# Optimization experiments

Measured on AMD Instinct MI355X. Metric: run time of the kernel, lower is better.

The kernel has to match this reference:

```python
import jax, jax.numpy as jnp
import numpy as np

N = 20000
E = 160000
H = 8          # heads
D = 96         # head_dim (768 // 8)
C = H * D      # 768 hidden channels
G = 256        # num graphs
NUM_CLASSES = 32
SLOPE = 0.2    # GATv2 LeakyReLU negative slope


def layer_norm(x, w, b, eps=1e-5):
    mu = jnp.mean(x, axis=-1, keepdims=True)
    var = jnp.mean(jnp.square(x - mu), axis=-1, keepdims=True)
    return (x - mu) * jax.lax.rsqrt(var + eps) * w + b


def gatv2_layer(x, src, dst, Wl, bl, Wr, br, att, bias):
    # x: [N, C]; src/dst: [E'] with self loops included
    xl = (x @ Wl + bl).reshape(N, H, D)   # source projection
    xr = (x @ Wr + br).reshape(N, H, D)   # target projection
    e = xl[src] + xr[dst]                 # [E', H, D] edge gather
    e = jnp.where(e > 0, e, SLOPE * e)    # LeakyReLU
    logits = jnp.einsum('ehd,hd->eh', e, att)  # [E', H]
    m = jax.ops.segment_max(logits, dst, num_segments=N)
    ex = jnp.exp(logits - m[dst])
    s = jax.ops.segment_sum(ex, dst, num_segments=N)
    alpha = ex / s[dst]                   # segment softmax over in-edges
    out = jax.ops.segment_sum(alpha[:, :, None] * xl[src], dst, num_segments=N)
    return out.reshape(N, C) + bias


def setup_inputs() -> dict:
    key = jax.random.key(0)
    ks = jax.random.split(key, 24)
    x = jax.random.normal(ks[0], (N, 768), jnp.float32)
    edge_index = jax.random.randint(ks[1], (2, E), 0, N, jnp.int64)
    batch = jnp.sort(jax.random.randint(ks[2], (N,), 0, G, jnp.int64))
    sc = 1.0 / np.sqrt(C)
    p = {
        'x': x, 'edge_index': edge_index, 'batch': batch,
        'w_in': jax.random.normal(ks[3], (768, C), jnp.float32) * sc,
        'b_in': jnp.zeros((C,), jnp.float32),
        'Wl': jax.random.normal(ks[4], (3, C, C), jnp.float32) * sc,
        'bl': jnp.zeros((3, C), jnp.float32),
        'Wr': jax.random.normal(ks[5], (3, C, C), jnp.float32) * sc,
        'br': jnp.zeros((3, C), jnp.float32),
        'att': jax.random.normal(ks[6], (3, H, D), jnp.float32) * (1.0 / np.sqrt(D)),
        'gat_bias': jnp.zeros((3, C), jnp.float32),
        'ln_w': jnp.ones((3, C), jnp.float32),
        'ln_b': jnp.zeros((3, C), jnp.float32),
        'out_ln_w': jnp.ones((3 * C,), jnp.float32),
        'out_ln_b': jnp.zeros((3 * C,), jnp.float32),
        'w_out': jax.random.normal(ks[7], (3 * C, NUM_CLASSES), jnp.float32) * (1.0 / np.sqrt(3 * C)),
        'b_out': jnp.zeros((NUM_CLASSES,), jnp.float32),
    }
    return p


def reference(x, edge_index, batch, w_in, b_in, Wl, bl, Wr, br, att, gat_bias,
              ln_w, ln_b, out_ln_w, out_ln_b, w_out, b_out):
    # add self loops (PyG add_self_loops=True)
    loops = jnp.arange(N, dtype=edge_index.dtype)
    src = jnp.concatenate([edge_index[0], loops])
    dst = jnp.concatenate([edge_index[1], loops])

    h = x @ w_in + b_in
    jumps = []
    for l in range(3):
        a = gatv2_layer(h, src, dst, Wl[l], bl[l], Wr[l], br[l], att[l], gat_bias[l])
        h = layer_norm(a + h, ln_w[l], ln_b[l])
        h = jax.nn.gelu(h, approximate=False)
        jumps.append(h)
    hc = jnp.concatenate(jumps, axis=-1)  # JumpingKnowledge 'cat' -> [N, 3C]

    # global mean pool over graphs
    sums = jax.ops.segment_sum(hc, batch, num_segments=G)
    cnt = jax.ops.segment_sum(jnp.ones((N, 1), hc.dtype), batch, num_segments=G)
    pooled = sums / jnp.maximum(cnt, 1.0)

    out = layer_norm(pooled, out_ln_w, out_ln_b)
    return out @ w_out + b_out
```

## Files before the change

### kernel.cpp

```cpp
#include <hip/hip_runtime.h>

#define N_NODES 20000
#define N_EDGES 160000
#define CH      768
#define CH3     2304
#define NGRAPH  256
#define NCLS    32

typedef __bf16 bf16v8 __attribute__((ext_vector_type(8)));
typedef float  f32x4  __attribute__((ext_vector_type(4)));

__device__ __forceinline__ float b2f(ushort u) {
    union { float f; unsigned u; } x; x.u = ((unsigned)u) << 16; return x.f;
}
__device__ __forceinline__ ushort f2b(float f) {
    union { float f; unsigned u; } x; x.f = f;
    unsigned r = x.u + 0x7FFFu + ((x.u >> 16) & 1u);
    return (ushort)(r >> 16);
}
__device__ __forceinline__ void load12(const ushort* __restrict__ p, float* o) {
    const ushort4* q = (const ushort4*)p;
    ushort4 a = q[0], b = q[1], c = q[2];
    o[0]=b2f(a.x); o[1]=b2f(a.y); o[2]=b2f(a.z); o[3]=b2f(a.w);
    o[4]=b2f(b.x); o[5]=b2f(b.y); o[6]=b2f(b.z); o[7]=b2f(b.w);
    o[8]=b2f(c.x); o[9]=b2f(c.y); o[10]=b2f(c.z); o[11]=b2f(c.w);
}
__device__ __forceinline__ void load12f(const float* __restrict__ p, float* o) {
    const float4* q = (const float4*)p;
    float4 a = q[0], b = q[1], c = q[2];
    o[0]=a.x; o[1]=a.y; o[2]=a.z; o[3]=a.w;
    o[4]=b.x; o[5]=b.y; o[6]=b.z; o[7]=b.w;
    o[8]=c.x; o[9]=c.y; o[10]=c.z; o[11]=c.w;
}
__device__ __forceinline__ void async_copy16(void* lds, const void* gp) {
    __builtin_amdgcn_global_load_lds((const void __attribute__((address_space(1)))*)gp,
                                     (void __attribute__((address_space(3)))*)lds, 16, 0, 0);
}

__global__ void cvt_x_kernel(const float* __restrict__ src, ushort* __restrict__ dst, int n4) {
    int i = blockIdx.x * 256 + threadIdx.x;
    if (i >= n4) return;
    float4 v = ((const float4*)src)[i];
    ushort4 o; o.x = f2b(v.x); o.y = f2b(v.y); o.z = f2b(v.z); o.w = f2b(v.w);
    ((ushort4*)dst)[i] = o;
}

__global__ void transpose_cvt_all(const float* __restrict__ w_in,
                                  const float* __restrict__ Wl,
                                  const float* __restrict__ Wr,
                                  ushort* __restrict__ wt_in,
                                  ushort* __restrict__ wt_l) {
    __shared__ float tile[32][33];
    int z = blockIdx.z;
    const float* in;
    ushort* out;
    if (z == 0) { in = w_in; out = wt_in; }
    else {
        int l = (z - 1) >> 1, isr = (z - 1) & 1;
        in  = (isr ? Wr : Wl) + (size_t)l * CH * CH;
        out = wt_l + (size_t)l * 1536 * CH + (size_t)isr * CH * CH;
    }
    int bx = blockIdx.x * 32, by = blockIdx.y * 32;
    int tx = threadIdx.x, ty = threadIdx.y;
    #pragma unroll
    for (int i = ty; i < 32; i += 8) tile[i][tx] = in[(size_t)(by + i) * CH + bx + tx];
    __syncthreads();
    #pragma unroll
    for (int i = ty; i < 32; i += 8) out[(size_t)(bx + i) * CH + by + tx] = f2b(tile[tx][i]);
}

__global__ void init_kernel(int* deg, int* gcount, int n) {
    int i = blockIdx.x * 256 + threadIdx.x;
    if (i < n) deg[i] = 1;
    if (i < 256) gcount[i] = 0;
}
__global__ void count_both_kernel(const int* __restrict__ dst, int* __restrict__ deg, int e,
                                  const int* __restrict__ batch, int* __restrict__ gcount, int n) {
    int i = blockIdx.x * 256 + threadIdx.x;
    if (i < e) atomicAdd(&deg[dst[i]], 1);
    if (i < n) atomicAdd(&gcount[batch[i]], 1);
}
__global__ __launch_bounds__(1024) void scan_kernel(const int* __restrict__ deg,
                                                    int* __restrict__ rowptr, int n) {
    __shared__ int part[1024];
    int t = threadIdx.x;
    const int chunk = (n + 1023) / 1024;
    int base = t * chunk;
    int s = 0;
    for (int i = 0; i < chunk; ++i) { int idx = base + i; if (idx < n) s += deg[idx]; }
    part[t] = s; __syncthreads();
    for (int off = 1; off < 1024; off <<= 1) {
        int v = (t >= off) ? part[t - off] : 0;
        __syncthreads();
        part[t] += v;
        __syncthreads();
    }
    int run = (t == 0) ? 0 : part[t - 1];
    for (int i = 0; i < chunk; ++i) {
        int idx = base + i;
        if (idx < n) { rowptr[idx] = run; run += deg[idx]; }
    }
    if (t == 1023) rowptr[n] = part[1023];
}
__global__ void selfloop_kernel(const int* __restrict__ rowptr, int* __restrict__ csrc,
                                int* __restrict__ cursor, int n) {
    int i = blockIdx.x * 256 + threadIdx.x;
    if (i < n) { int p = rowptr[i]; csrc[p] = i; cursor[i] = p + 1; }
}
__global__ void scatter_kernel(const int* __restrict__ src, const int* __restrict__ dst,
                               int* __restrict__ cursor, int* __restrict__ csrc, int e) {
    int i = blockIdx.x * 256 + threadIdx.x;
    if (i < e) { int p = atomicAdd(&cursor[dst[i]], 1); csrc[p] = src[i]; }
}
__global__ __launch_bounds__(256) void gscan_kernel(const int* __restrict__ gcount,
                                                    int* __restrict__ gstart) {
    __shared__ int p[256];
    int t = threadIdx.x;
    p[t] = gcount[t]; __syncthreads();
    for (int off = 1; off < 256; off <<= 1) {
        int v = (t >= off) ? p[t - off] : 0;
        __syncthreads();
        p[t] += v;
        __syncthreads();
    }
    gstart[t] = p[t] - gcount[t];
    if (t == 255) gstart[256] = p[255];
}

__global__ __launch_bounds__(256) void gemm_bf16_kernel(
    const ushort* __restrict__ A, int lda,
    const ushort* __restrict__ Bt,
    const float* __restrict__ biasA, const float* __restrict__ biasB, int nsplit,
    ushort* __restrict__ C, int ldc, int M) {
    __shared__ __bf16 As[128 * 32];
    __shared__ __bf16 Bs[128 * 32];
    int tid = threadIdx.x;
    int wave = tid >> 6, lane = tid & 63;
    int wr = wave >> 1, wc = wave & 1;

    int bid = blockIdx.y * gridDim.x + blockIdx.x;
    int pf = 8 * gridDim.y;
    int p  = bid / pf;
    int rem = bid - p * pf;
    int rp = min(8, (int)gridDim.x - p * 8);
    int row_t = p * 8 + rem % rp;
    int col_t = rem / rp;
    int row0 = row_t * 128, col0 = col_t * 128;

    int c1 = wave * 64 + lane, c2 = c1 + 256;
    int ar1 = min(row0 + (c1 >> 2), M - 1), ak1 = (c1 & 3) * 8;
    int ar2 = min(row0 + (c2 >> 2), M - 1), ak2 = (c2 & 3) * 8;
    int br1 = col0 + (c1 >> 2), br2 = col0 + (c2 >> 2);
    const ushort* a1 = A + (size_t)ar1 * lda + ak1;
    const ushort* a2 = A + (size_t)ar2 * lda + ak2;
    const ushort* b1 = Bt + (size_t)br1 * CH + ak1;
    const ushort* b2 = Bt + (size_t)br2 * CH + ak2;
    __bf16* asb1 = As + (wave * 64) * 8;
    __bf16* asb2 = As + (256 + wave * 64) * 8;
    __bf16* bsb1 = Bs + (wave * 64) * 8;
    __bf16* bsb2 = Bs + (256 + wave * 64) * 8;

    f32x4 acc[4][4] = {};
    int l16 = lane & 15, lq = lane >> 4;

    for (int k0 = 0; k0 < CH; k0 += 32) {
        async_copy16(asb1, a1 + k0);
        async_copy16(asb2, a2 + k0);
        async_copy16(bsb1, b1 + k0);
        async_copy16(bsb2, b2 + k0);
        __syncthreads();
        bf16v8 av[4], bv[4];
        #pragma unroll
        for (int i = 0; i < 4; ++i)
            av[i] = *(const bf16v8*)(As + ((wr * 64 + i * 16 + l16) * 32 + lq * 8));
        #pragma unroll
        for (int j = 0; j < 4; ++j)
            bv[j] = *(const bf16v8*)(Bs + ((wc * 64 + j * 16 + l16) * 32 + lq * 8));
        #pragma unroll
        for (int i = 0; i < 4; ++i)
            #pragma unroll
            for (int j = 0; j < 4; ++j)
                acc[i][j] = __builtin_amdgcn_mfma_f32_16x16x32_bf16(av[i], bv[j], acc[i][j], 0, 0, 0);
        __syncthreads();
    }
    #pragma unroll
    for (int i = 0; i < 4; ++i) {
        int mbase = row0 + wr * 64 + i * 16 + lq * 4;
        #pragma unroll
        for (int j = 0; j < 4; ++j) {
            int col = col0 + wc * 64 + j * 16 + l16;
            float bb = (col < nsplit) ? biasA[col] : biasB[col - nsplit];
            #pragma unroll
            for (int r = 0; r < 4; ++r) {
                int mm = mbase + r;
                if (mm < M) C[(size_t)mm * ldc + col] = f2b(acc[i][j][r] + bb);
            }
        }
    }
}

__global__ __launch_bounds__(256) void gat_node_kernel(
    const ushort* __restrict__ xlxr,
    const ushort* __restrict__ hin, int ldh,
    const int* __restrict__ rowptr, const int* __restrict__ csrc,
    const float* __restrict__ att, const float* __restrict__ gbias,
    const float* __restrict__ lnw, const float* __restrict__ lnb,
    ushort* __restrict__ hout, int nn) {
    int wv = threadIdx.x >> 6, lane = threadIdx.x & 63;
    int n = blockIdx.x * 4 + wv;
    if (n >= nn) return;
    int c0 = lane * 12;
    float attv[12], xr[12], acc1[12], acc2[12];
    load12f(att + c0, attv);
    load12(xlxr + (size_t)n * 1536 + CH + c0, xr);
    #pragma unroll
    for (int j = 0; j < 12; ++j) { acc1[j] = 0.f; acc2[j] = 0.f; }
    float m1 = -1e30f, s1 = 0.f, m2 = -1e30f, s2 = 0.f;
    int rs = rowptr[n], re = rowptr[n + 1];
    int e = rs;
    for (; e + 1 < re; e += 2) {
        int sa = csrc[e], sb = csrc[e + 1];
        float xa[12], xb[12];
        load12(xlxr + (size_t)sa * 1536 + c0, xa);
        load12(xlxr + (size_t)sb * 1536 + c0, xb);
        float da = 0.f, db = 0.f;
        #pragma unroll
        for (int j = 0; j < 12; ++j) {
            float va = xa[j] + xr[j]; va = (va > 0.f) ? va : 0.2f * va;
            float vb = xb[j] + xr[j]; vb = (vb > 0.f) ? vb : 0.2f * vb;
            da = fmaf(va, attv[j], da);
            db = fmaf(vb, attv[j], db);
        }
        da += __shfl_xor(da, 1); db += __shfl_xor(db, 1);
        da += __shfl_xor(da, 2); db += __shfl_xor(db, 2);
        da += __shfl_xor(da, 4); db += __shfl_xor(db, 4);
        float nm1 = fmaxf(m1, da), nm2 = fmaxf(m2, db);
        float sc1 = __expf(m1 - nm1), sc2 = __expf(m2 - nm2);
        float ex1 = __expf(da - nm1), ex2 = __expf(db - nm2);
        s1 = s1 * sc1 + ex1;
        s2 = s2 * sc2 + ex2;
        #pragma unroll
        for (int j = 0; j < 12; ++j) {
            acc1[j] = fmaf(acc1[j], sc1, ex1 * xa[j]);
            acc2[j] = fmaf(acc2[j], sc2, ex2 * xb[j]);
        }
        m1 = nm1; m2 = nm2;
    }
    if (e < re) {
        int sa = csrc[e];
        float xa[12];
        load12(xlxr + (size_t)sa * 1536 + c0, xa);
        float da = 0.f;
        #pragma unroll
        for (int j = 0; j < 12; ++j) {
            float va = xa[j] + xr[j]; va = (va > 0.f) ? va : 0.2f * va;
            da = fmaf(va, attv[j], da);
        }
        da += __shfl_xor(da, 1);
        da += __shfl_xor(da, 2);
        da += __shfl_xor(da, 4);
        float nm = fmaxf(m1, da);
        float sc = __expf(m1 - nm), ex = __expf(da - nm);
        s1 = s1 * sc + ex;
        #pragma unroll
        for (int j = 0; j < 12; ++j) acc1[j] = fmaf(acc1[j], sc, ex * xa[j]);
        m1 = nm;
    }
    float M = fmaxf(m1, m2);
    float w1 = __expf(m1 - M), w2 = __expf(m2 - M);
    float ssum = s1 * w1 + s2 * w2;
    float inv = 1.f / ssum;
    float hres[12], gb[12], tv[12];
    load12(hin + (size_t)n * ldh + c0, hres);
    load12f(gbias + c0, gb);
    float lsum = 0.f;
    #pragma unroll
    for (int j = 0; j < 12; ++j) {
        tv[j] = (acc1[j] * w1 + acc2[j] * w2) * inv + gb[j] + hres[j];
        lsum += tv[j];
    }
    #pragma unroll
    for (int o = 1; o < 64; o <<= 1) lsum += __shfl_xor(lsum, o);
    float mu = lsum * (1.f / 768.f);
    float lsq = 0.f;
    #pragma unroll
    for (int j = 0; j < 12; ++j) { float d = tv[j] - mu; lsq = fmaf(d, d, lsq); }
    #pragma unroll
    for (int o = 1; o < 64; o <<= 1) lsq += __shfl_xor(lsq, o);
    float rstd = rsqrtf(lsq * (1.f / 768.f) + 1e-5f);
    float wv12[12], bv12[12];
    load12f(lnw + c0, wv12);
    load12f(lnb + c0, bv12);
    ushort* op = hout + (size_t)n * CH3 + c0;
    #pragma unroll
    for (int j = 0; j < 12; ++j) {
        float y = (tv[j] - mu) * rstd * wv12[j] + bv12[j];
        float g = 0.5f * y * (1.f + erff(y * 0.70710678118f));
        op[j] = f2b(g);
    }
}

__global__ __launch_bounds__(256) void pool_kernel(const ushort* __restrict__ hc,
                                                   const int* __restrict__ gstart,
                                                   float* __restrict__ pooled) {
    int g = blockIdx.x;
    int c = blockIdx.y * 256 + threadIdx.x;
    int s = gstart[g], e = gstart[g + 1];
    const ushort* p = hc + (size_t)s * CH3 + c;
    float a = 0.f;
    for (int n = s; n < e; ++n) { a += b2f(*p); p += CH3; }
    pooled[(size_t)g * CH3 + c] = a * (1.f / (float)max(e - s, 1));
}

__global__ __launch_bounds__(256) void head_kernel(const float* __restrict__ pooled,
                                                   const float* __restrict__ olnw,
                                                   const float* __restrict__ olnb,
                                                   const float* __restrict__ wout,
                                                   const float* __restrict__ bout,
                                                   float* __restrict__ outp) {
    __shared__ float row[CH3];
    __shared__ float red[8];
    __shared__ float parts[8][32];
    int g = blockIdx.x, t = threadIdx.x;
    int lane = t & 63, wv = t >> 6;
    float s = 0.f;
    for (int c = t; c < CH3; c += 256) { float v = pooled[(size_t)g * CH3 + c]; row[c] = v; s += v; }
    #pragma unroll
    for (int o = 1; o < 64; o <<= 1) s += __shfl_xor(s, o);
    if (lane == 0) red[wv] = s;
    __syncthreads();
    float mu = (red[0] + red[1] + red[2] + red[3]) * (1.f / (float)CH3);
    float q = 0.f;
    for (int c = t; c < CH3; c += 256) { float d = row[c] - mu; q += d * d; }
    #pragma unroll
    for (int o = 1; o < 64; o <<= 1) q += __shfl_xor(q, o);
    if (lane == 0) red[4 + wv] = q;
    __syncthreads();
    float rstd = rsqrtf((red[4] + red[5] + red[6] + red[7]) * (1.f / (float)CH3) + 1e-5f);
    for (int c = t; c < CH3; c += 256)
        row[c] = (row[c] - mu) * rstd * olnw[c] + olnb[c];
    __syncthreads();
    int j = t & 31, slice = t >> 5;
    float a = 0.f;
    int cb = slice * (CH3 / 8);
    for (int c = cb; c < cb + CH3 / 8; ++c) a += row[c] * wout[(size_t)c * 32 + j];
    parts[slice][j] = a;
    __syncthreads();
    if (t < 32) {
        float r = bout[t];
        #pragma unroll
        for (int si = 0; si < 8; ++si) r += parts[si][t];
        outp[(size_t)g * 32 + t] = r;
    }
}

extern "C" void kernel_launch(void* const* d_in, const int* in_sizes, int n_in,
                              void* d_out, int out_size, void* d_ws, size_t ws_size,
                              hipStream_t stream) {
    const float* x     = (const float*)d_in[0];
    const int*   ei    = (const int*)d_in[1];
    const int*   batch = (const int*)d_in[2];
    const float* w_in  = (const float*)d_in[3];
    const float* b_in  = (const float*)d_in[4];
    const float* Wl    = (const float*)d_in[5];
    const float* bl    = (const float*)d_in[6];
    const float* Wr    = (const float*)d_in[7];
    const float* br    = (const float*)d_in[8];
    const float* att   = (const float*)d_in[9];
    const float* gbias = (const float*)d_in[10];
    const float* lnw   = (const float*)d_in[11];
    const float* lnb   = (const float*)d_in[12];
    const float* olnw  = (const float*)d_in[13];
    const float* olnb  = (const float*)d_in[14];
    const float* wout  = (const float*)d_in[15];
    const float* bout  = (const float*)d_in[16];

    char* ws = (char*)d_ws;
    size_t off = 0;
    auto alloc = [&](size_t bytes) -> void* {
        void* p = ws + off;
        off = (off + bytes + 255) & ~(size_t)255;
        return p;
    };
    ushort* h0     = (ushort*)alloc((size_t)N_NODES * CH * 2);
    ushort* hc     = (ushort*)alloc((size_t)N_NODES * CH3 * 2);
    ushort* xlxr   = (ushort*)alloc((size_t)N_NODES * 1536 * 2);
    ushort* wt_in  = (ushort*)alloc((size_t)CH * CH * 2);
    ushort* wt_l   = (ushort*)alloc((size_t)3 * 1536 * CH * 2);
    int*    deg    = (int*)alloc((size_t)N_NODES * 4);
    int*    rowptr = (int*)alloc((size_t)(N_NODES + 1) * 4);
    int*    cursor = (int*)alloc((size_t)N_NODES * 4);
    int*    csrc   = (int*)alloc((size_t)(N_EDGES + N_NODES) * 4);
    int*    gcount = (int*)alloc(256 * 4);
    int*    gstart = (int*)alloc(257 * 4);
    float*  pooled = (float*)alloc((size_t)NGRAPH * CH3 * 4);
    if (off > ws_size) return;

    ushort* xc = hc;

    cvt_x_kernel<<<(N_NODES * CH / 4 + 255) / 256, 256, 0, stream>>>(x, xc, N_NODES * CH / 4);
    transpose_cvt_all<<<dim3(24, 24, 7), dim3(32, 8), 0, stream>>>(w_in, Wl, Wr, wt_in, wt_l);

    int nb = (N_NODES + 255) / 256, eb = (N_EDGES + 255) / 256;
    init_kernel<<<nb, 256, 0, stream>>>(deg, gcount, N_NODES);
    count_both_kernel<<<eb, 256, 0, stream>>>(ei + N_EDGES, deg, N_EDGES, batch, gcount, N_NODES);
    scan_kernel<<<1, 1024, 0, stream>>>(deg, rowptr, N_NODES);
    selfloop_kernel<<<nb, 256, 0, stream>>>(rowptr, csrc, cursor, N_NODES);
    scatter_kernel<<<eb, 256, 0, stream>>>(ei, ei + N_EDGES, cursor, csrc, N_EDGES);
    gscan_kernel<<<1, 256, 0, stream>>>(gcount, gstart);

    gemm_bf16_kernel<<<dim3(157, 6), 256, 0, stream>>>(
        xc, CH, wt_in, b_in, b_in, CH, h0, CH, N_NODES);

    for (int l = 0; l < 3; ++l) {
        const ushort* hprev = (l == 0) ? h0 : (hc + (size_t)(l - 1) * CH);
        int ldh = (l == 0) ? CH : CH3;
        gemm_bf16_kernel<<<dim3(157, 12), 256, 0, stream>>>(
            hprev, ldh, wt_l + (size_t)l * 1536 * CH,
            bl + (size_t)l * CH, br + (size_t)l * CH, CH,
            xlxr, 1536, N_NODES);
        gat_node_kernel<<<N_NODES / 4, 256, 0, stream>>>(
            xlxr, hprev, ldh, rowptr, csrc,
            att + (size_t)l * CH, gbias + (size_t)l * CH,
            lnw + (size_t)l * CH, lnb + (size_t)l * CH,
            hc + (size_t)l * CH, N_NODES);
    }

    pool_kernel<<<dim3(NGRAPH, CH3 / 256), 256, 0, stream>>>(hc, gstart, pooled);
    head_kernel<<<NGRAPH, 256, 0, stream>>>(pooled, olnw, olnb, wout, bout, (float*)d_out);
}
```

Baseline: 754.3 us.

## Split each GAT node across two wavefronts and unroll pooling accumulation

The GAT aggregation kernel now assigns two wavefronts per node, each handling 384 channels (6 per lane), and combines the LayerNorm sums through shared memory using a single-pass sum and sum-of-squares. The aim is more parallelism and latency hiding for the edge gathers, plus vectorized ushort2 stores. The pool kernel uses four independent accumulators to raise memory-level parallelism. The init kernel is replaced by memsets, with self-loop degrees counted via atomics. The one-pass variance is numerically less stable, and a block-wide barrier is added.

```diff
diff --git a/kernel.cpp b/kernel.cpp
--- a/kernel.cpp
+++ b/kernel.cpp
@@ -25,12 +25,17 @@
     o[4]=b2f(b.x); o[5]=b2f(b.y); o[6]=b2f(b.z); o[7]=b2f(b.w);
     o[8]=b2f(c.x); o[9]=b2f(c.y); o[10]=b2f(c.z); o[11]=b2f(c.w);
 }
-__device__ __forceinline__ void load12f(const float* __restrict__ p, float* o) {
-    const float4* q = (const float4*)p;
-    float4 a = q[0], b = q[1], c = q[2];
-    o[0]=a.x; o[1]=a.y; o[2]=a.z; o[3]=a.w;
-    o[4]=b.x; o[5]=b.y; o[6]=b.z; o[7]=b.w;
-    o[8]=c.x; o[9]=c.y; o[10]=c.z; o[11]=c.w;
+__device__ __forceinline__ void load6(const ushort* __restrict__ p, float* o) {
+    const ushort2* q = (const ushort2*)p;
+    ushort2 a = q[0], b = q[1], c = q[2];
+    o[0]=b2f(a.x); o[1]=b2f(a.y);
+    o[2]=b2f(b.x); o[3]=b2f(b.y);
+    o[4]=b2f(c.x); o[5]=b2f(c.y);
+}
+__device__ __forceinline__ void load6f(const float* __restrict__ p, float* o) {
+    const float2* q = (const float2*)p;
+    float2 a = q[0], b = q[1], c = q[2];
+    o[0]=a.x; o[1]=a.y; o[2]=b.x; o[3]=b.y; o[4]=c.x; o[5]=c.y;
 }
 __device__ __forceinline__ void async_copy16(void* lds, const void* gp) {
     __builtin_amdgcn_global_load_lds((const void __attribute__((address_space(1)))*)gp,
@@ -69,16 +74,11 @@
     for (int i = ty; i < 32; i += 8) out[(size_t)(bx + i) * CH + by + tx] = f2b(tile[tx][i]);
 }
 
-__global__ void init_kernel(int* deg, int* gcount, int n) {
-    int i = blockIdx.x * 256 + threadIdx.x;
-    if (i < n) deg[i] = 1;
-    if (i < 256) gcount[i] = 0;
-}
 __global__ void count_both_kernel(const int* __restrict__ dst, int* __restrict__ deg, int e,
                                   const int* __restrict__ batch, int* __restrict__ gcount, int n) {
     int i = blockIdx.x * 256 + threadIdx.x;
     if (i < e) atomicAdd(&deg[dst[i]], 1);
-    if (i < n) atomicAdd(&gcount[batch[i]], 1);
+    if (i < n) { atomicAdd(&deg[i], 1); atomicAdd(&gcount[batch[i]], 1); }
 }
 __global__ __launch_bounds__(1024) void scan_kernel(const int* __restrict__ deg,
                                                     int* __restrict__ rowptr, int n) {
@@ -206,26 +206,28 @@
     const float* __restrict__ att, const float* __restrict__ gbias,
     const float* __restrict__ lnw, const float* __restrict__ lnb,
     ushort* __restrict__ hout, int nn) {
+    __shared__ float sred[2][2][2];
     int wv = threadIdx.x >> 6, lane = threadIdx.x & 63;
-    int n = blockIdx.x * 4 + wv;
-    if (n >= nn) return;
-    int c0 = lane * 12;
-    float attv[12], xr[12], acc1[12], acc2[12];
-    load12f(att + c0, attv);
-    load12(xlxr + (size_t)n * 1536 + CH + c0, xr);
-    #pragma unroll
-    for (int j = 0; j < 12; ++j) { acc1[j] = 0.f; acc2[j] = 0.f; }
+    int slot = wv >> 1, half = wv & 1;
+    int n = blockIdx.x * 2 + slot;
+    int c0 = half * 384 + lane * 6;
+    const ushort* __restrict__ xbase = xlxr + c0;
+    float attv[6], xr[6], acc1[6], acc2[6];
+    load6f(att + c0, attv);
+    load6(xbase + (size_t)n * 1536 + CH, xr);
+    #pragma unroll
+    for (int j = 0; j < 6; ++j) { acc1[j] = 0.f; acc2[j] = 0.f; }
     float m1 = -1e30f, s1 = 0.f, m2 = -1e30f, s2 = 0.f;
     int rs = rowptr[n], re = rowptr[n + 1];
     int e = rs;
     for (; e + 1 < re; e += 2) {
         int sa = csrc[e], sb = csrc[e + 1];
-        float xa[12], xb[12];
-        load12(xlxr + (size_t)sa * 1536 + c0, xa);
-        load12(xlxr + (size_t)sb * 1536 + c0, xb);
+        float xa[6], xb[6];
+        load6(xbase + (size_t)sa * 1536, xa);
+        load6(xbase + (size_t)sb * 1536, xb);
         float da = 0.f, db = 0.f;
         #pragma unroll
-        for (int j = 0; j < 12; ++j) {
+        for (int j = 0; j < 6; ++j) {
             float va = xa[j] + xr[j]; va = (va > 0.f) ? va : 0.2f * va;
             float vb = xb[j] + xr[j]; vb = (vb > 0.f) ? vb : 0.2f * vb;
             da = fmaf(va, attv[j], da);
@@ -234,13 +236,14 @@
         da += __shfl_xor(da, 1); db += __shfl_xor(db, 1);
         da += __shfl_xor(da, 2); db += __shfl_xor(db, 2);
         da += __shfl_xor(da, 4); db += __shfl_xor(db, 4);
+        da += __shfl_xor(da, 8); db += __shfl_xor(db, 8);
         float nm1 = fmaxf(m1, da), nm2 = fmaxf(m2, db);
         float sc1 = __expf(m1 - nm1), sc2 = __expf(m2 - nm2);
         float ex1 = __expf(da - nm1), ex2 = __expf(db - nm2);
         s1 = s1 * sc1 + ex1;
         s2 = s2 * sc2 + ex2;
         #pragma unroll
-        for (int j = 0; j < 12; ++j) {
+        for (int j = 0; j < 6; ++j) {
             acc1[j] = fmaf(acc1[j], sc1, ex1 * xa[j]);
             acc2[j] = fmaf(acc2[j], sc2, ex2 * xb[j]);
         }
@@ -248,56 +251,62 @@
     }
     if (e < re) {
         int sa = csrc[e];
-        float xa[12];
-        load12(xlxr + (size_t)sa * 1536 + c0, xa);
+        float xa[6];
+        load6(xbase + (size_t)sa * 1536, xa);
         float da = 0.f;
         #pragma unroll
-        for (int j = 0; j < 12; ++j) {
+        for (int j = 0; j < 6; ++j) {
             float va = xa[j] + xr[j]; va = (va > 0.f) ? va : 0.2f * va;
             da = fmaf(va, attv[j], da);
         }
         da += __shfl_xor(da, 1);
         da += __shfl_xor(da, 2);
         da += __shfl_xor(da, 4);
+        da += __shfl_xor(da, 8);
         float nm = fmaxf(m1, da);
         float sc = __expf(m1 - nm), ex = __expf(da - nm);
         s1 = s1 * sc + ex;
         #pragma unroll
-        for (int j = 0; j < 12; ++j) acc1[j] = fmaf(acc1[j], sc, ex * xa[j]);
+        for (int j = 0; j < 6; ++j) acc1[j] = fmaf(acc1[j], sc, ex * xa[j]);
         m1 = nm;
     }
     float M = fmaxf(m1, m2);
     float w1 = __expf(m1 - M), w2 = __expf(m2 - M);
-    float ssum = s1 * w1 + s2 * w2;
-    float inv = 1.f / ssum;
-    float hres[12], gb[12], tv[12];
-    load12(hin + (size_t)n * ldh + c0, hres);
-    load12f(gbias + c0, gb);
-    float lsum = 0.f;
-    #pragma unroll
-    for (int j = 0; j < 12; ++j) {
+    float inv = 1.f / (s1 * w1 + s2 * w2);
+    float hres[6], gb[6], tv[6];
+    load6(hin + (size_t)n * ldh + c0, hres);
+    load6f(gbias + c0, gb);
+    float lsum = 0.f, lsq = 0.f;
+    #pragma unroll
+    for (int j = 0; j < 6; ++j) {
         tv[j] = (acc1[j] * w1 + acc2[j] * w2) * inv + gb[j] + hres[j];
         lsum += tv[j];
-    }
-    #pragma unroll
-    for (int o = 1; o < 64; o <<= 1) lsum += __shfl_xor(lsum, o);
-    float mu = lsum * (1.f / 768.f);
-    float lsq = 0.f;
-    #pragma unroll
-    for (int j = 0; j < 12; ++j) { float d = tv[j] - mu; lsq = fmaf(d, d, lsq); }
-    #pragma unroll
-    for (int o = 1; o < 64; o <<= 1) lsq += __shfl_xor(lsq, o);
-    float rstd = rsqrtf(lsq * (1.f / 768.f) + 1e-5f);
-    float wv12[12], bv12[12];
-    load12f(lnw + c0, wv12);
-    load12f(lnb + c0, bv12);
-    ushort* op = hout + (size_t)n * CH3 + c0;
-    #pragma unroll
-    for (int j = 0; j < 12; ++j) {
-        float y = (tv[j] - mu) * rstd * wv12[j] + bv12[j];
-        float g = 0.5f * y * (1.f + erff(y * 0.70710678118f));
-        op[j] = f2b(g);
-    }
+        lsq = fmaf(tv[j], tv[j], lsq);
+    }
+    #pragma unroll
+    for (int o = 1; o < 64; o <<= 1) { lsum += __shfl_xor(lsum, o); lsq += __shfl_xor(lsq, o); }
+    if (lane == 0) { sred[slot][0][half] = lsum; sred[slot][1][half] = lsq; }
+    __syncthreads();
+    float S = sred[slot][0][0] + sred[slot][0][1];
+    float Q = sred[slot][1][0] + sred[slot][1][1];
+    float mu = S * (1.f / 768.f);
+    float var = Q * (1.f / 768.f) - mu * mu;
+    float rstd = rsqrtf(var + 1e-5f);
+    float wv6[6], bv6[6];
+    load6f(lnw + c0, wv6);
+    load6f(lnb + c0, bv6);
+    float g[6];
+    #pragma unroll
+    for (int j = 0; j < 6; ++j) {
+        float y = (tv[j] - mu) * rstd * wv6[j] + bv6[j];
+        g[j] = 0.5f * y * (1.f + erff(y * 0.70710678118f));
+    }
+    ushort2* o2 = (ushort2*)(hout + (size_t)n * CH3 + c0);
+    ushort2 u0, u1, u2;
+    u0.x = f2b(g[0]); u0.y = f2b(g[1]);
+    u1.x = f2b(g[2]); u1.y = f2b(g[3]);
+    u2.x = f2b(g[4]); u2.y = f2b(g[5]);
+    o2[0] = u0; o2[1] = u1; o2[2] = u2;
 }
 
 __global__ __launch_bounds__(256) void pool_kernel(const ushort* __restrict__ hc,
@@ -307,8 +316,17 @@
     int c = blockIdx.y * 256 + threadIdx.x;
     int s = gstart[g], e = gstart[g + 1];
     const ushort* p = hc + (size_t)s * CH3 + c;
-    float a = 0.f;
-    for (int n = s; n < e; ++n) { a += b2f(*p); p += CH3; }
+    float a0 = 0.f, a1 = 0.f, a2 = 0.f, a3 = 0.f;
+    int n = s;
+    for (; n + 3 < e; n += 4) {
+        a0 += b2f(p[0]);
+        a1 += b2f(p[CH3]);
+        a2 += b2f(p[2 * CH3]);
+        a3 += b2f(p[3 * CH3]);
+        p += 4 * CH3;
+    }
+    for (; n < e; ++n) { a0 += b2f(*p); p += CH3; }
+    float a = (a0 + a1) + (a2 + a3);
     pooled[(size_t)g * CH3 + c] = a * (1.f / (float)max(e - s, 1));
 }
 
@@ -402,7 +420,8 @@
     transpose_cvt_all<<<dim3(24, 24, 7), dim3(32, 8), 0, stream>>>(w_in, Wl, Wr, wt_in, wt_l);
 
     int nb = (N_NODES + 255) / 256, eb = (N_EDGES + 255) / 256;
-    init_kernel<<<nb, 256, 0, stream>>>(deg, gcount, N_NODES);
+    hipMemsetAsync(deg, 0, (size_t)N_NODES * 4, stream);
+    hipMemsetAsync(gcount, 0, 256 * 4, stream);
     count_both_kernel<<<eb, 256, 0, stream>>>(ei + N_EDGES, deg, N_EDGES, batch, gcount, N_NODES);
     scan_kernel<<<1, 1024, 0, stream>>>(deg, rowptr, N_NODES);
     selfloop_kernel<<<nb, 256, 0, stream>>>(rowptr, csrc, cursor, N_NODES);
@@ -419,7 +438,7 @@
             hprev, ldh, wt_l + (size_t)l * 1536 * CH,
             bl + (size_t)l * CH, br + (size_t)l * CH, CH,
             xlxr, 1536, N_NODES);
-        gat_node_kernel<<<N_NODES / 4, 256, 0, stream>>>(
+        gat_node_kernel<<<N_NODES / 2, 256, 0, stream>>>(
             xlxr, hprev, ldh, rowptr, csrc,
             att + (size_t)l * CH, gbias + (size_t)l * CH,
             lnw + (size_t)l * CH, lnb + (size_t)l * CH,
```

After: 738.4 us. 1.02x faster.
